# Kernel optimization log

Hardware: AMD Instinct MI355X
Metric: run time of the kernel (lower is better)

Reference implementation:

```python
import jax, jax.numpy as jnp
import numpy as np

B, N, F = 512, 32, 16          # batch graphs, nodes per graph, node_obs dim (last col = entity type)
H, E, NE, L = 128, 16, 3, 2    # hidden, embedding_size, num_embeddings, embed_layer_N
MAX_EDGE_DIST = 1.0


def layer_norm(x, g, b, eps=1e-5):
    mu = jnp.mean(x, axis=-1, keepdims=True)
    var = jnp.mean((x - mu) ** 2, axis=-1, keepdims=True)
    return (x - mu) / jnp.sqrt(var + eps) * g + b


def setup_inputs() -> dict:
    key = jax.random.key(0)
    ks = jax.random.split(key, 12)
    feats = jax.random.normal(ks[0], (B, N, F - 1), jnp.float32)
    ent = jax.random.randint(ks[1], (B, N), 0, NE).astype(jnp.float32)
    node_obs = jnp.concatenate([feats, ent[..., None]], axis=-1)
    adj = jax.random.uniform(ks[2], (B, N, N), jnp.float32, 0.0, 2.0)
    adj = adj * (1.0 - jnp.eye(N, dtype=jnp.float32))  # no self distance
    agent_id = jax.random.randint(ks[3], (B, 1), 0, N)
    D0 = (F - 1) + E + 1  # node feats + entity embed + edge_attr
    s = 0.05
    return dict(
        node_obs=node_obs, adj=adj, agent_id=agent_id,
        entity_embed=jax.random.normal(ks[4], (NE, E), jnp.float32) * s,
        lin1_w=jax.random.normal(ks[5], (D0, H), jnp.float32) * s, lin1_b=jnp.zeros(H, jnp.float32),
        ln1_g=jnp.ones(H, jnp.float32), ln1_b=jnp.zeros(H, jnp.float32),
        linh_w=jax.random.normal(ks[6], (L, H, H), jnp.float32) * s, linh_b=jnp.zeros((L, H), jnp.float32),
        lnh_g=jnp.ones((L, H), jnp.float32), lnh_b=jnp.zeros((L, H), jnp.float32),
        fc2a_w=jax.random.normal(ks[7], (H, H), jnp.float32) * s, fc2a_b=jnp.zeros(H, jnp.float32),
        fc2b_w=jax.random.normal(ks[8], (H, 1), jnp.float32) * s, fc2b_b=jnp.zeros(1, jnp.float32),
        fc3_w=jax.random.normal(ks[9], (H, H), jnp.float32) * s, fc3_b=jnp.zeros(H, jnp.float32),
        ln3_g=jnp.ones(H, jnp.float32), ln3_b=jnp.zeros(H, jnp.float32),
        fc4_w=jax.random.normal(ks[10], (H, H), jnp.float32) * s, fc4_b=jnp.zeros(H, jnp.float32),
        ln4_g=jnp.ones(H, jnp.float32), ln4_b=jnp.zeros(H, jnp.float32),
    )


def reference(node_obs, adj, agent_id, entity_embed,
              lin1_w, lin1_b, ln1_g, ln1_b,
              linh_w, linh_b, lnh_g, lnh_b,
              fc2a_w, fc2a_b, fc2b_w, fc2b_b,
              fc3_w, fc3_b, ln3_g, ln3_b,
              fc4_w, fc4_b, ln4_g, ln4_b):
    # processAdj: edge (r -> c) exists where 0 < adj[r,c] < max_edge_dist, edge_attr = adj value
    mask = ((adj > 0) & (adj < MAX_EDGE_DIST)).astype(adj.dtype)      # [B,N,N] (r=source, c=target)
    e = adj * mask
    # EmbedConv.message: x_j features + entity embedding + edge_attr -> MLP
    feat_j = node_obs[..., :-1]                                       # [B,N,F-1]
    ent = node_obs[..., -1].astype(jnp.int32)                         # [B,N]
    xj = jnp.concatenate([feat_j, entity_embed[ent]], axis=-1)        # [B,N,F-1+E]
    src = jnp.broadcast_to(xj[:, :, None, :], (B, N, N, xj.shape[-1]))
    pair = jnp.concatenate([src, e[..., None]], axis=-1)              # [B,r,c,D0]
    m = layer_norm(jax.nn.relu(pair @ lin1_w + lin1_b), ln1_g, ln1_b) # [B,r,c,H]
    for l in range(linh_w.shape[0]):
        m = layer_norm(jax.nn.relu(m @ linh_w[l] + linh_b[l]), lnh_g[l], lnh_b[l])
    # scatter-add aggregation at target node c (masked sum over sources r)
    h = jnp.einsum('brc,brch->bch', mask, m)                          # [B,N,H]
    hf = h.reshape(B * N, -1)
    # attention: fc2 then softmax over ALL batched-graph nodes (dim=0, as in source)
    alpha = jax.nn.softmax(jax.nn.relu(hf @ fc2a_w + fc2a_b) @ fc2b_w + fc2b_b, axis=0)  # [B*N,1]
    v = layer_norm(jax.nn.relu(hf @ fc3_w + fc3_b), ln3_g, ln3_b)
    x = layer_norm(jax.nn.relu((alpha * v) @ fc4_w + fc4_b), ln4_g, ln4_b)
    x = x.reshape(B, N, -1)
    # graph_aggr == 'node': gather agent's node features
    out = x[jnp.arange(B), agent_id[:, 0].astype(jnp.int32)]          # [B,H]
    return out
```

## Files before the change

### kernel.cpp

```cpp
#include <hip/hip_runtime.h>
#include <hip/hip_bf16.h>


typedef __attribute__((ext_vector_type(8))) __bf16 bf16x8;
typedef __attribute__((ext_vector_type(4))) float  f32x4;
typedef __attribute__((ext_vector_type(2))) float  f32x2;

__device__ float g_bf[256];

__device__ __forceinline__ unsigned short f2bf(float f) {
  union { float f; unsigned u; } v; v.f = f;
  unsigned u = v.u;
  u += 0x7FFFu + ((u >> 16) & 1u);
  return (unsigned short)(u >> 16);
}

__device__ __forceinline__ unsigned pk2bf(float a, float b) {
  union { __hip_bfloat162 h; unsigned u; } cv;
  cv.h = __float22bfloat162_rn(make_float2(a, b));
  return cv.u;
}

__device__ __forceinline__ bf16x8 lds_frag(const unsigned short* p) {
  union { uint4 u; bf16x8 v; } x;
  x.u = *(const uint4*)p;
  return x.v;
}

__device__ __forceinline__ f32x4 mfma16(bf16x8 a, bf16x8 b, f32x4 c) {
  return __builtin_amdgcn_mfma_f32_16x16x32_bf16(a, b, c, 0, 0, 0);
}

__device__ __forceinline__ float dpp_add16(float x) {
  union { float f; int i; } a, t;
  a.f = x;
  t.i = __builtin_amdgcn_update_dpp(0, a.i, 0xB1,  0xF, 0xF, true); a.f += t.f;
  t.i = __builtin_amdgcn_update_dpp(0, a.i, 0x4E,  0xF, 0xF, true); a.f += t.f;
  t.i = __builtin_amdgcn_update_dpp(0, a.i, 0x141, 0xF, 0xF, true); a.f += t.f;
  t.i = __builtin_amdgcn_update_dpp(0, a.i, 0x140, 0xF, 0xF, true); a.f += t.f;
  return a.f;
}

__device__ __forceinline__ void gll16(const void* g, void* l) {
  __builtin_amdgcn_global_load_lds(
      (const __attribute__((address_space(1))) unsigned int*)(unsigned long long)g,
      (__attribute__((address_space(3))) unsigned int*)(unsigned int)(unsigned long long)l,
      16, 0, 0);
}

__device__ __forceinline__ void stage18432(const char* g, char* l, int tid) {
  int off = tid * 16;
  gll16(g + off,         l + off);
  gll16(g + off + 4096,  l + off + 4096);
  gll16(g + off + 8192,  l + off + 8192);
  gll16(g + off + 12288, l + off + 12288);
  if (tid < 128) gll16(g + off + 16384, l + off + 16384);
}

#define WS_HB    0
#define WS_HSEL  4194304
#define WS_SWS   4456448
#define WS_STATS 4521984
#define WS_XJB   4522240
#define WS_WT0P  5570816
#define WS_W1P   5581056
#define WS_W2P   5617920
#define WS_WT3P  5654784

#define PREP_N0 524288
#define PREP_N1 (PREP_N0 + 5120)
#define PREP_N2 (PREP_N1 + 36864)
#define PREP_N3 (PREP_N2 + 17408)
#define PREP_N4 (PREP_N3 + 256)
#define PREP_N5 (PREP_N4 + 2)

__global__ void k_prep(const float* __restrict__ node_obs, const float* __restrict__ ent_emb,
                       const float* __restrict__ lin1_w, const float* __restrict__ linh_w,
                       const float* __restrict__ fc2a_w,
                       const float* __restrict__ ln1_g, const float* __restrict__ ln1_b,
                       const float* __restrict__ lnh_g, const float* __restrict__ lnh_b,
                       const float* __restrict__ linh_b,
                       char* __restrict__ ws) {
  int idx = blockIdx.x * 256 + threadIdx.x;
  unsigned short* xjb  = (unsigned short*)(ws + WS_XJB);
  unsigned short* WT0p = (unsigned short*)(ws + WS_WT0P);
  unsigned short* W1p  = (unsigned short*)(ws + WS_W1P);
  unsigned short* W2p  = (unsigned short*)(ws + WS_W2P);
  unsigned short* WT3p = (unsigned short*)(ws + WS_WT3P);
  if (idx < PREP_N0) {
    int row = idx >> 5, k = idx & 31;
    float val;
    if (k < 15) val = node_obs[row * 16 + k];
    else if (k < 31) {
      int ent = (int)node_obs[row * 16 + 15];
      val = ent_emb[ent * 16 + (k - 15)];
    } else val = 0.f;
    xjb[idx] = f2bf(val);
  } else if (idx < PREP_N1) {
    int r = idx - PREP_N0;
    int n = r / 40, kk = r - n * 40;
    WT0p[n * 40 + kk] = (kk < 32) ? f2bf(lin1_w[kk * 128 + n]) : (unsigned short)0;
  } else if (idx < PREP_N2) {
    int r = idx - PREP_N1;
    int l = r / 18432; r -= l * 18432;
    int h = r / 9216;  r -= h * 9216;
    int n = r / 72;    int kk = r - n * 72;
    unsigned short v = 0;
    if (kk < 64) {
      int p  = h * 64 + kk;
      int ok = 32 * (p >> 5) + 16 * (p & 1) + ((p >> 1) & 15);
      float g = l ? lnh_g[ok] : ln1_g[ok];
      v = f2bf(g * linh_w[l * 16384 + ok * 128 + n]);
    }
    (l ? W2p : W1p)[h * 9216 + n * 72 + kk] = v;
  } else if (idx < PREP_N3) {
    int r = idx - PREP_N2;
    int n = r / 136, kk = r - n * 136;
    unsigned short v = 0;
    if (kk < 128) {
      int ok = 32 * (kk >> 5) + 16 * (kk & 1) + ((kk >> 1) & 15);
      v = f2bf(fc2a_w[ok * 128 + n]);
    }
    WT3p[n * 136 + kk] = v;
  } else if (idx < PREP_N4) {
    int r = idx - PREP_N3;
    int which = r >> 7, n = r & 127;
    const float* be = which ? lnh_b : ln1_b;
    const float* w  = linh_w + which * 16384 + n;
    float a = linh_b[which * 128 + n];
#pragma unroll 8
    for (int k = 0; k < 128; ++k) a += be[k] * w[k * 128];
    g_bf[which * 128 + n] = a;
  } else if (idx < PREP_N5) {
    ((unsigned*)(ws + WS_STATS + 16))[idx - PREP_N4] = 0u;
  }
}

__global__ __launch_bounds__(256)
void k_mask(const float* __restrict__ adj, char* __restrict__ ws) {
  const int tid = threadIdx.x, lane = tid & 63, wv = tid >> 6;
  int p = blockIdx.x * 256 + tid;
  int b = p >> 5, c = p & 31;
  int cnt = 0;
#pragma unroll 8
  for (int r = 0; r < 32; ++r) {
    float a = adj[(b * 32 + r) * 32 + c];
    cnt += (a > 0.f && a < 1.f) ? 1 : 0;
  }
  const bool big = cnt > 16;
  unsigned long long bal = __ballot(big);
  __shared__ unsigned sb[4], ss[4];
  __shared__ unsigned base_b, base_s;
  if (lane == 0) {
    unsigned nb = (unsigned)__popcll(bal);
    sb[wv] = nb; ss[wv] = 64u - nb;
  }
  __syncthreads();
  if (tid == 0) {
    unsigned tb = 0, ts = 0;
#pragma unroll
    for (int i = 0; i < 4; ++i) {
      unsigned t = sb[i]; sb[i] = tb; tb += t;
      t = ss[i]; ss[i] = ts; ts += t;
    }
    unsigned* tcnt = (unsigned*)(ws + WS_STATS + 16);
    base_b = atomicAdd(&tcnt[0], tb);
    base_s = atomicAdd(&tcnt[1], ts);
  }
  __syncthreads();
  unsigned long long mlow = (1ull << lane) - 1ull;
  unsigned short* bigl = (unsigned short*)(ws + WS_SWS);
  unsigned short* smal = bigl + 16384;
  if (big) {
    unsigned rk = base_b + sb[wv] + (unsigned)__popcll(bal & mlow);
    bigl[rk] = (unsigned short)p;
  } else {
    unsigned rk = base_s + ss[wv] + (unsigned)__popcll(~bal & mlow);
    smal[rk] = (unsigned short)p;
  }
}

__device__ __forceinline__ void bias_acc(f32x4 (&acc)[2][8],
                                         const float* __restrict__ gb, int li) {
#pragma unroll
  for (int tj = 0; tj < 8; ++tj) {
    float b = gb[tj * 16 + li];
#pragma unroll
    for (int ti = 0; ti < 2; ++ti)
#pragma unroll
      for (int q = 0; q < 4; ++q) acc[ti][tj][q] = b;
  }
}

__device__ __forceinline__ void epilogue_store(f32x4 (&acc)[2][8],
    unsigned short* Xs, int wv, int li, int quad) {
  const f32x2 z2 = {0.f, 0.f};
#pragma unroll
  for (int ti = 0; ti < 2; ++ti) {
#pragma unroll
    for (int rp = 0; rp < 2; ++rp) {
      f32x2 vv[8], s1 = {0.f, 0.f}, s2 = {0.f, 0.f};
#pragma unroll
      for (int tj = 0; tj < 8; ++tj) {
        f32x2 x = { acc[ti][tj][2 * rp], acc[ti][tj][2 * rp + 1] };
        x = __builtin_elementwise_max(x, z2);
        vv[tj] = x; s1 += x; s2 += x * x;
      }
      f32x2 S1 = { dpp_add16(s1.x), dpp_add16(s1.y) };
      f32x2 S2 = { dpp_add16(s2.x), dpp_add16(s2.y) };
      f32x2 mean = S1 * 0.0078125f;
      f32x2 var  = S2 * 0.0078125f - mean * mean;
      f32x2 inv  = { rsqrtf(var.x + 1e-5f), rsqrtf(var.y + 1e-5f) };
      f32x2 c0   = -mean * inv;
      int r0 = 32 * wv + ti * 16 + quad * 4 + 2 * rp;
      unsigned* d0 = (unsigned*)(Xs + r0 * 136);
      unsigned* d1 = (unsigned*)(Xs + (r0 + 1) * 136);
#pragma unroll
      for (int g4 = 0; g4 < 4; ++g4) {
        f32x2 oa = vv[2 * g4]     * inv + c0;
        f32x2 ob = vv[2 * g4 + 1] * inv + c0;
        d0[g4 * 16 + li] = pk2bf(oa.x, ob.x);
        d1[g4 * 16 + li] = pk2bf(oa.y, ob.y);
      }
    }
  }
}

__device__ __forceinline__ void agg_reduce_write(float (&T)[8], float Q, float NM,
    const float* __restrict__ gg, const float* __restrict__ gbe,
    int pair, const int* __restrict__ agent_id, char* __restrict__ ws,
    int li, int quad) {
#pragma unroll
  for (int tj = 0; tj < 8; ++tj) {
    T[tj] += __shfl_xor(T[tj], 16);
    T[tj] += __shfl_xor(T[tj], 32);
  }
  Q += __shfl_xor(Q, 16); Q += __shfl_xor(Q, 32);
  if (quad != 0 || pair < 0) return;
  float cs[8];
#pragma unroll
  for (int tj = 0; tj < 8; ++tj) {
    int col = tj * 16 + li;
    cs[tj] = gg[col] * (T[tj] - Q) + NM * gbe[col];
  }
  unsigned* hb32 = (unsigned*)((unsigned short*)(ws + WS_HB) + pair * 128);
#pragma unroll
  for (int g4 = 0; g4 < 4; ++g4)
    hb32[g4 * 16 + li] = pk2bf(cs[2 * g4], cs[2 * g4 + 1]);
  int b = pair >> 5;
  if ((pair & 31) == agent_id[b]) {
    float* hs = (float*)(ws + WS_HSEL) + b * 128;
#pragma unroll
    for (int tj = 0; tj < 8; ++tj) hs[tj * 16 + li] = cs[tj];
  }
}

__device__ __forceinline__ void epilogue_agg2(f32x4 (&acc)[2][8],
    const float* __restrict__ gg, const float* __restrict__ gbe,
    int big, int cnt0, int cnt1, int p0, int p1,
    const int* __restrict__ agent_id, char* __restrict__ ws,
    int li, int quad) {
  const f32x2 z2 = {0.f, 0.f};
  float T0[8], T1[8], Q0 = 0.f, Q1 = 0.f;
#pragma unroll
  for (int ti = 0; ti < 2; ++ti) {
    f32x2 Tp[8];
#pragma unroll
    for (int tj = 0; tj < 8; ++tj) Tp[tj] = z2;
    f32x2 Qp = z2;
    float lim   = big ? (float)(cnt0 + cnt1) : (float)(ti ? cnt1 : cnt0);
    float rbase = (float)((big ? ti * 16 : 0) + quad * 4);
#pragma unroll
    for (int rp = 0; rp < 2; ++rp) {
      f32x2 vv[8], s1 = z2, s2 = z2;
#pragma unroll
      for (int tj = 0; tj < 8; ++tj) {
        f32x2 x = { acc[ti][tj][2 * rp], acc[ti][tj][2 * rp + 1] };
        x = __builtin_elementwise_max(x, z2);
        vv[tj] = x; s1 += x; s2 += x * x;
      }
      f32x2 S1 = { dpp_add16(s1.x), dpp_add16(s1.y) };
      f32x2 S2 = { dpp_add16(s2.x), dpp_add16(s2.y) };
      f32x2 mean = S1 * 0.0078125f;
      f32x2 var  = S2 * 0.0078125f - mean * mean;
      f32x2 inv  = { rsqrtf(var.x + 1e-5f), rsqrtf(var.y + 1e-5f) };
      float r0f = rbase + (float)(2 * rp);
      f32x2 mk = { (r0f < lim) ? 1.f : 0.f, (r0f + 1.f < lim) ? 1.f : 0.f };
      f32x2 u = mk * inv;
      Qp += u * mean;
#pragma unroll
      for (int tj = 0; tj < 8; ++tj) Tp[tj] += u * vv[tj];
    }
    if (ti == 0) {
#pragma unroll
      for (int tj = 0; tj < 8; ++tj) T0[tj] = Tp[tj].x + Tp[tj].y;
      Q0 = Qp.x + Qp.y;
    } else {
#pragma unroll
      for (int tj = 0; tj < 8; ++tj) T1[tj] = Tp[tj].x + Tp[tj].y;
      Q1 = Qp.x + Qp.y;
    }
  }
  if (big) {
#pragma unroll
    for (int tj = 0; tj < 8; ++tj) T0[tj] += T1[tj];
    Q0 += Q1;
    agg_reduce_write(T0, Q0, (float)(cnt0 + cnt1), gg, gbe, p0, agent_id, ws, li, quad);
  } else {
    agg_reduce_write(T0, Q0, (float)cnt0, gg, gbe, p0, agent_id, ws, li, quad);
    agg_reduce_write(T1, Q1, (float)cnt1, gg, gbe, p1, agent_id, ws, li, quad);
  }
}

#define SMP_W 34816
#define SMP_TOTAL 53248

__device__ __forceinline__ void mfma_half(f32x4 (&acc)[2][8],
    const unsigned short* Xs, const unsigned short* Wh,
    int xoff, int wv, int li, int quad) {
#pragma unroll
  for (int s = 0; s < 2; ++s) {
    bf16x8 a0 = lds_frag(Xs + (32 * wv + li) * 136 + xoff + s * 32 + quad * 8);
    bf16x8 a1 = lds_frag(Xs + (32 * wv + 16 + li) * 136 + xoff + s * 32 + quad * 8);
#pragma unroll
    for (int tj = 0; tj < 8; ++tj) {
      bf16x8 bb = lds_frag(Wh + (tj * 16 + li) * 72 + s * 32 + quad * 8);
      acc[0][tj] = mfma16(a0, bb, acc[0][tj]);
      acc[1][tj] = mfma16(a1, bb, acc[1][tj]);
    }
  }
}

__global__ __launch_bounds__(256, 3)
void k_pair(const float* __restrict__ adj, const int* __restrict__ agent_id,
            const float* __restrict__ lin1_b,
            const float* __restrict__ lnh_g, const float* __restrict__ lnh_b,
            char* __restrict__ ws) {
  __shared__ alignas(16) char smem[SMP_TOTAL];
  unsigned short* Xs = (unsigned short*)smem;
  unsigned short* Wh = (unsigned short*)(smem + SMP_W);

  const unsigned short* xjb = (const unsigned short*)(ws + WS_XJB);
  const char* WT0p = ws + WS_WT0P;
  const char* W1p  = ws + WS_W1P;
  const char* W2p  = ws + WS_W2P;

  const int tid  = threadIdx.x;
  const int lane = tid & 63, li = lane & 15, quad = lane >> 4, wv = tid >> 6;

  const unsigned* tcnt = (const unsigned*)(ws + WS_STATS + 16);
  const int n_big = (int)tcnt[0], n_small = (int)tcnt[1];
  const int n_task = n_big + ((n_small + 1) >> 1);
  if ((int)(blockIdx.x * 4) >= n_task) return;
  const int slot = blockIdx.x * 4 + wv;
  const unsigned short* bigl = (const unsigned short*)(ws + WS_SWS);
  const unsigned short* smal = bigl + 16384;
  int p0 = -1, p1 = -1, big = 0;
  if (slot < n_big) { p0 = bigl[slot]; big = 1; }
  else if (slot < n_task) {
    int j = slot - n_big;
    p0 = smal[2 * j];
    if (2 * j + 1 < n_small) p1 = smal[2 * j + 1];
  }

  const int r = lane & 31, hh = lane >> 5;
  int pp = big ? (hh ? -1 : p0) : (hh ? p1 : p0);
  float a_val = 0.f;
  if (pp >= 0) a_val = adj[(((pp >> 5) * 32 + r) * 32) + (pp & 31)];
  const bool live = (a_val > 0.f) && (a_val < 1.f);
  unsigned long long bal = __ballot(live);
  unsigned hm = hh ? (unsigned)(bal >> 32) : (unsigned)bal;
  int pre = __popc(hm & ((1u << r) - 1u));
  int slot_in = big ? pre : (hh * 16 + pre);
  int cnt0, cnt1;
  if (big) { int ca = __popc((unsigned)bal); cnt0 = ca < 16 ? ca : 16; cnt1 = ca - cnt0; }
  else     { cnt0 = __popc((unsigned)bal); cnt1 = __popc((unsigned)(bal >> 32)); }
  unsigned* scr = (unsigned*)(smem + 10240 + wv * 128);
  if (live) scr[slot_in] = (unsigned)r;

  {
    const uint4* src = (const uint4*)xjb;
    char* tile = smem + wv * 2560;
    int j0 = lane >> 2, j1 = 16 + (lane >> 2), pt = lane & 3;
    int ca = cnt0 + cnt1;
    bool v0 = j0 < (big ? ca : cnt0);
    bool v1 = big ? (j1 < ca) : ((j1 - 16) < cnt1);
    int b0 = (p0 < 0 ? 0 : p0 >> 5);
    int b1 = (p1 < 0 ? 0 : p1 >> 5);
    int sb1 = big ? b0 : b1;
    unsigned sr0 = v0 ? scr[j0] : 0u;
    unsigned sr1 = v1 ? scr[j1] : 0u;
    uint4 z4 = {0u, 0u, 0u, 0u};
    uint4 q0 = v0 ? src[(b0 * 32 + (int)sr0) * 4 + pt] : z4;
    uint4 q1 = v1 ? src[(sb1 * 32 + (int)sr1) * 4 + pt] : z4;
    *(uint4*)(tile + j0 * 80 + pt * 16) = q0;
    *(uint4*)(tile + j1 * 80 + pt * 16) = q1;
    if (live) ((unsigned short*)(tile + slot_in * 80))[31] = f2bf(a_val);
  }
  {
    int off = tid * 16;
    gll16(WT0p + off, smem + SMP_W + off);
    gll16(WT0p + off + 4096, smem + SMP_W + off + 4096);
    if (tid < 128) gll16(WT0p + off + 8192, smem + SMP_W + off + 8192);
  }
  __syncthreads();

  f32x4 acc[2][8];

  bias_acc(acc, lin1_b, li);
  {
    const unsigned short* xt = (const unsigned short*)(smem + wv * 2560);
    bf16x8 a0 = lds_frag(xt + li * 40 + quad * 8);
    bf16x8 a1 = lds_frag(xt + (li + 16) * 40 + quad * 8);
#pragma unroll
    for (int tj = 0; tj < 8; ++tj) {
      bf16x8 bb = lds_frag(Wh + (tj * 16 + li) * 40 + quad * 8);
      acc[0][tj] = mfma16(a0, bb, acc[0][tj]);
      acc[1][tj] = mfma16(a1, bb, acc[1][tj]);
    }
  }
  __syncthreads();
  stage18432(W1p, smem + SMP_W, tid);
  epilogue_store(acc, Xs, wv, li, quad);
  __syncthreads();

  bias_acc(acc, g_bf, li);
  mfma_half(acc, Xs, Wh, 0, wv, li, quad);
  __syncthreads();
  stage18432(W1p + 18432, smem + SMP_W, tid);
  __syncthreads();
  mfma_half(acc, Xs, Wh, 64, wv, li, quad);
  __syncthreads();
  stage18432(W2p, smem + SMP_W, tid);
  epilogue_store(acc, Xs, wv, li, quad);
  __syncthreads();

  bias_acc(acc, g_bf + 128, li);
  mfma_half(acc, Xs, Wh, 0, wv, li, quad);
  __syncthreads();
  stage18432(W2p + 18432, smem + SMP_W, tid);
  __syncthreads();
  mfma_half(acc, Xs, Wh, 64, wv, li, quad);

  epilogue_agg2(acc, lnh_g + 128, lnh_b + 128, big, cnt0, cnt1, p0, p1,
                agent_id, ws, li, quad);
}

#define SC_TOTAL 70656
__global__ __launch_bounds__(256, 2)
void k_score(const char* __restrict__ ws,
             const float* __restrict__ fc2a_b, const float* __restrict__ fc2b_w,
             const float* __restrict__ fc2b_b) {
  __shared__ alignas(16) char smem[SC_TOTAL];
  unsigned short* Xs = (unsigned short*)smem;
  unsigned short* Ws = (unsigned short*)(smem + 34816);
  float* P = (float*)(smem + 69632);
  const int tid = threadIdx.x;
  const int row0 = blockIdx.x * 128;
  const uint4* hb4 = (const uint4*)(ws + WS_HB);
  const char* WT3p = ws + WS_WT3P;
  float* sws = (float*)((char*)ws + WS_SWS);

  for (int i = tid; i < 2048; i += 256) {
    int row = i >> 4, ch = i & 15;
    uint4 v = hb4[(row0 + row) * 16 + ch];
    *(uint4*)(Xs + row * 136 + ch * 8) = v;
  }
  {
    int off = tid * 16;
#pragma unroll
    for (int it = 0; it < 8; ++it) gll16(WT3p + off + it * 4096, smem + 34816 + off + it * 4096);
    if (tid < 128) gll16(WT3p + off + 32768, smem + 34816 + off + 32768);
  }
  if (tid < 128) { P[tid] = fc2a_b[tid]; P[128 + tid] = fc2b_w[tid]; }
  __syncthreads();

  const int lane = tid & 63, li = lane & 15, quad = lane >> 4, wv = tid >> 6;
  f32x4 acc[2][8];
#pragma unroll
  for (int ti = 0; ti < 2; ++ti)
#pragma unroll
    for (int tj = 0; tj < 8; ++tj)
#pragma unroll
      for (int q = 0; q < 4; ++q) acc[ti][tj][q] = 0.f;
#pragma unroll
  for (int s = 0; s < 4; ++s) {
    bf16x8 a0 = lds_frag(Xs + (32 * wv + li) * 136 + s * 32 + quad * 8);
    bf16x8 a1 = lds_frag(Xs + (32 * wv + 16 + li) * 136 + s * 32 + quad * 8);
#pragma unroll
    for (int tj = 0; tj < 8; ++tj) {
      bf16x8 bb = lds_frag(Ws + (tj * 16 + li) * 136 + s * 32 + quad * 8);
      acc[0][tj] = mfma16(a0, bb, acc[0][tj]);
      acc[1][tj] = mfma16(a1, bb, acc[1][tj]);
    }
  }
  float bs[8], w2[8];
#pragma unroll
  for (int tj = 0; tj < 8; ++tj) {
    bs[tj] = P[tj * 16 + li];
    w2[tj] = P[128 + tj * 16 + li];
  }
  float b2 = fc2b_b[0];
#pragma unroll
  for (int ti = 0; ti < 2; ++ti) {
#pragma unroll
    for (int rg = 0; rg < 4; ++rg) {
      float t = 0.f;
#pragma unroll
      for (int tj = 0; tj < 8; ++tj) {
        float x = acc[ti][tj][rg] + bs[tj];
        x = fmaxf(x, 0.f);
        t += x * w2[tj];
      }
#pragma unroll
      for (int m = 1; m < 16; m <<= 1) t += __shfl_xor(t, m);
      if (li == 0) sws[row0 + 32 * wv + ti * 16 + quad * 4 + rg] = t + b2;
    }
  }
}

__global__ __launch_bounds__(1024)
void k_stats(char* __restrict__ ws) {
  const float* sws = (const float*)(ws + WS_SWS);
  float* stats = (float*)(ws + WS_STATS);
  __shared__ float red[1024];
  const int tid = threadIdx.x;
  float m = -3.0e38f;
  for (int i = tid; i < 16384; i += 1024) m = fmaxf(m, sws[i]);
  red[tid] = m;
  __syncthreads();
  for (int st = 512; st > 0; st >>= 1) {
    if (tid < st) red[tid] = fmaxf(red[tid], red[tid + st]);
    __syncthreads();
  }
  float mx = red[0];
  __syncthreads();
  float sm = 0.f;
  for (int i = tid; i < 16384; i += 1024) sm += __expf(sws[i] - mx);
  red[tid] = sm;
  __syncthreads();
  for (int st = 512; st > 0; st >>= 1) {
    if (tid < st) red[tid] += red[tid + st];
    __syncthreads();
  }
  if (tid == 0) { stats[0] = mx; stats[1] = red[0]; }
}

__global__ __launch_bounds__(128)
void k_final(const char* __restrict__ ws, const int* __restrict__ agent_id,
             const float* __restrict__ fc3_w, const float* __restrict__ fc3_b,
             const float* __restrict__ ln3_g, const float* __restrict__ ln3_b,
             const float* __restrict__ fc4_w, const float* __restrict__ fc4_b,
             const float* __restrict__ ln4_g, const float* __restrict__ ln4_b,
             float* __restrict__ out) {
  const float* hsel  = (const float*)(ws + WS_HSEL);
  const float* sws   = (const float*)(ws + WS_SWS);
  const float* stats = (const float*)(ws + WS_STATS);
  __shared__ float xrow[128];
  __shared__ float red[8];
  const int tid = threadIdx.x;
  const int b = blockIdx.x;
  xrow[tid] = hsel[b * 128 + tid];
  __syncthreads();
  float t = fc3_b[tid];
  for (int k = 0; k < 128; ++k) t += xrow[k] * fc3_w[k * 128 + tid];
  t = fmaxf(t, 0.f);
  float s1 = t, s2 = t * t;
#pragma unroll
  for (int m = 1; m < 64; m <<= 1) { s1 += __shfl_xor(s1, m); s2 += __shfl_xor(s2, m); }
  if ((tid & 63) == 0) { red[(tid >> 6) * 2] = s1; red[(tid >> 6) * 2 + 1] = s2; }
  __syncthreads();
  s1 = red[0] + red[2]; s2 = red[1] + red[3];
  float mean = s1 * 0.0078125f;
  float var  = s2 * 0.0078125f - mean * mean;
  float inv  = rsqrtf(var + 1e-5f);
  float v = (t - mean) * inv * ln3_g[tid] + ln3_b[tid];
  float alpha = __expf(sws[b * 32 + agent_id[b]] - stats[0]) / stats[1];
  __syncthreads();
  xrow[tid] = alpha * v;
  __syncthreads();
  float x = fc4_b[tid];
  for (int k = 0; k < 128; ++k) x += xrow[k] * fc4_w[k * 128 + tid];
  x = fmaxf(x, 0.f);
  s1 = x; s2 = x * x;
#pragma unroll
  for (int m = 1; m < 64; m <<= 1) { s1 += __shfl_xor(s1, m); s2 += __shfl_xor(s2, m); }
  if ((tid & 63) == 0) { red[4 + (tid >> 6) * 2] = s1; red[5 + (tid >> 6) * 2] = s2; }
  __syncthreads();
  s1 = red[4] + red[6]; s2 = red[5] + red[7];
  mean = s1 * 0.0078125f;
  var  = s2 * 0.0078125f - mean * mean;
  inv  = rsqrtf(var + 1e-5f);
  out[b * 128 + tid] = (x - mean) * inv * ln4_g[tid] + ln4_b[tid];
}

extern "C" void kernel_launch(void* const* d_in, const int* in_sizes, int n_in,
                              void* d_out, int out_size, void* d_ws, size_t ws_size,
                              hipStream_t stream) {
  (void)in_sizes; (void)n_in; (void)out_size; (void)ws_size;
  const float* node_obs = (const float*)d_in[0];
  const float* adj      = (const float*)d_in[1];
  const int*   agent_id = (const int*)d_in[2];
  const float* ent_emb  = (const float*)d_in[3];
  const float* lin1_w   = (const float*)d_in[4];
  const float* lin1_b   = (const float*)d_in[5];
  const float* ln1_g    = (const float*)d_in[6];
  const float* ln1_beta = (const float*)d_in[7];
  const float* linh_w   = (const float*)d_in[8];
  const float* linh_b   = (const float*)d_in[9];
  const float* lnh_g    = (const float*)d_in[10];
  const float* lnh_b    = (const float*)d_in[11];
  const float* fc2a_b   = (const float*)d_in[13];
  const float* fc2b_w   = (const float*)d_in[14];
  const float* fc2b_b   = (const float*)d_in[15];
  const float* fc3_w    = (const float*)d_in[16];
  const float* fc3_b    = (const float*)d_in[17];
  const float* ln3_g    = (const float*)d_in[18];
  const float* ln3_b    = (const float*)d_in[19];
  const float* fc4_w    = (const float*)d_in[20];
  const float* fc4_b    = (const float*)d_in[21];
  const float* ln4_g    = (const float*)d_in[22];
  const float* ln4_b    = (const float*)d_in[23];
  float* out = (float*)d_out;
  char* ws = (char*)d_ws;

  k_prep<<<(PREP_N5 + 255) / 256, 256, 0, stream>>>(node_obs, ent_emb, lin1_w, linh_w,
                                                    (const float*)d_in[12],
                                                    ln1_g, ln1_beta, lnh_g, lnh_b,
                                                    linh_b, ws);
  k_mask<<<64, 256, 0, stream>>>(adj, ws);
  k_pair<<<4096, 256, 0, stream>>>(adj, agent_id, lin1_b, lnh_g, lnh_b, ws);
  k_score<<<128, 256, 0, stream>>>(ws, fc2a_b, fc2b_w, fc2b_b);
  k_stats<<<1, 1024, 0, stream>>>(ws);
  k_final<<<512, 128, 0, stream>>>(ws, agent_id,
                                   fc3_w, fc3_b, ln3_g, ln3_b,
                                   fc4_w, fc4_b, ln4_g, ln4_b, out);
}
```

Baseline: 188.7 us.

## Make k_pair persistent with all MLP weights resident in LDS

k_pair becomes a persistent kernel: 256 blocks of 512 threads loop over tasks with a grid-stride loop. The three layer weight matrices are loaded into LDS once per block instead of being restaged in halves for every task. Each wave gets its own activation buffer, which removes the block-wide barriers between layers. Biases and LayerNorm parameters are hoisted into registers. The cost is about 154 KB of LDS per block, so only one block (8 waves) fits per CU, and load balancing relies on the grid stride.

```diff
diff --git a/kernel.cpp b/kernel.cpp
--- a/kernel.cpp
+++ b/kernel.cpp
@@ -46,15 +46,6 @@
       (const __attribute__((address_space(1))) unsigned int*)(unsigned long long)g,
       (__attribute__((address_space(3))) unsigned int*)(unsigned int)(unsigned long long)l,
       16, 0, 0);
-}
-
-__device__ __forceinline__ void stage18432(const char* g, char* l, int tid) {
-  int off = tid * 16;
-  gll16(g + off,         l + off);
-  gll16(g + off + 4096,  l + off + 4096);
-  gll16(g + off + 8192,  l + off + 8192);
-  gll16(g + off + 12288, l + off + 12288);
-  if (tid < 128) gll16(g + off + 16384, l + off + 16384);
 }
 
 #define WS_HB    0
@@ -180,20 +171,17 @@
   }
 }
 
-__device__ __forceinline__ void bias_acc(f32x4 (&acc)[2][8],
-                                         const float* __restrict__ gb, int li) {
-#pragma unroll
-  for (int tj = 0; tj < 8; ++tj) {
-    float b = gb[tj * 16 + li];
+__device__ __forceinline__ void bias_acc(f32x4 (&acc)[2][8], const float (&b8)[8]) {
+#pragma unroll
+  for (int tj = 0; tj < 8; ++tj)
 #pragma unroll
     for (int ti = 0; ti < 2; ++ti)
 #pragma unroll
-      for (int q = 0; q < 4; ++q) acc[ti][tj][q] = b;
-  }
+      for (int q = 0; q < 4; ++q) acc[ti][tj][q] = b8[tj];
 }
 
 __device__ __forceinline__ void epilogue_store(f32x4 (&acc)[2][8],
-    unsigned short* Xs, int wv, int li, int quad) {
+    unsigned short* Xw, int li, int quad) {
   const f32x2 z2 = {0.f, 0.f};
 #pragma unroll
   for (int ti = 0; ti < 2; ++ti) {
@@ -212,9 +200,9 @@
       f32x2 var  = S2 * 0.0078125f - mean * mean;
       f32x2 inv  = { rsqrtf(var.x + 1e-5f), rsqrtf(var.y + 1e-5f) };
       f32x2 c0   = -mean * inv;
-      int r0 = 32 * wv + ti * 16 + quad * 4 + 2 * rp;
-      unsigned* d0 = (unsigned*)(Xs + r0 * 136);
-      unsigned* d1 = (unsigned*)(Xs + (r0 + 1) * 136);
+      int r0 = ti * 16 + quad * 4 + 2 * rp;
+      unsigned* d0 = (unsigned*)(Xw + r0 * 136);
+      unsigned* d1 = (unsigned*)(Xw + (r0 + 1) * 136);
 #pragma unroll
       for (int g4 = 0; g4 < 4; ++g4) {
         f32x2 oa = vv[2 * g4]     * inv + c0;
@@ -227,7 +215,7 @@
 }
 
 __device__ __forceinline__ void agg_reduce_write(float (&T)[8], float Q, float NM,
-    const float* __restrict__ gg, const float* __restrict__ gbe,
+    const float (&gg8)[8], const float (&be8)[8],
     int pair, const int* __restrict__ agent_id, char* __restrict__ ws,
     int li, int quad) {
 #pragma unroll
@@ -239,10 +227,8 @@
   if (quad != 0 || pair < 0) return;
   float cs[8];
 #pragma unroll
-  for (int tj = 0; tj < 8; ++tj) {
-    int col = tj * 16 + li;
-    cs[tj] = gg[col] * (T[tj] - Q) + NM * gbe[col];
-  }
+  for (int tj = 0; tj < 8; ++tj)
+    cs[tj] = gg8[tj] * (T[tj] - Q) + NM * be8[tj];
   unsigned* hb32 = (unsigned*)((unsigned short*)(ws + WS_HB) + pair * 128);
 #pragma unroll
   for (int g4 = 0; g4 < 4; ++g4)
@@ -256,7 +242,7 @@
 }
 
 __device__ __forceinline__ void epilogue_agg2(f32x4 (&acc)[2][8],
-    const float* __restrict__ gg, const float* __restrict__ gbe,
+    const float (&gg8)[8], const float (&be8)[8],
     int big, int cnt0, int cnt1, int p0, int p1,
     const int* __restrict__ agent_id, char* __restrict__ ws,
     int li, int quad) {
@@ -305,145 +291,148 @@
 #pragma unroll
     for (int tj = 0; tj < 8; ++tj) T0[tj] += T1[tj];
     Q0 += Q1;
-    agg_reduce_write(T0, Q0, (float)(cnt0 + cnt1), gg, gbe, p0, agent_id, ws, li, quad);
+    agg_reduce_write(T0, Q0, (float)(cnt0 + cnt1), gg8, be8, p0, agent_id, ws, li, quad);
   } else {
-    agg_reduce_write(T0, Q0, (float)cnt0, gg, gbe, p0, agent_id, ws, li, quad);
-    agg_reduce_write(T1, Q1, (float)cnt1, gg, gbe, p1, agent_id, ws, li, quad);
-  }
-}
-
-#define SMP_W 34816
-#define SMP_TOTAL 53248
-
-__device__ __forceinline__ void mfma_half(f32x4 (&acc)[2][8],
-    const unsigned short* Xs, const unsigned short* Wh,
-    int xoff, int wv, int li, int quad) {
-#pragma unroll
-  for (int s = 0; s < 2; ++s) {
-    bf16x8 a0 = lds_frag(Xs + (32 * wv + li) * 136 + xoff + s * 32 + quad * 8);
-    bf16x8 a1 = lds_frag(Xs + (32 * wv + 16 + li) * 136 + xoff + s * 32 + quad * 8);
+    agg_reduce_write(T0, Q0, (float)cnt0, gg8, be8, p0, agent_id, ws, li, quad);
+    agg_reduce_write(T1, Q1, (float)cnt1, gg8, be8, p1, agent_id, ws, li, quad);
+  }
+}
+
+#define PL_W0    0
+#define PL_W1    10240
+#define PL_W2    47104
+#define PL_XS    83968
+#define PL_SCR   153600
+#define PL_TOTAL 154624
+
+__device__ __forceinline__ void mfma_fullK(f32x4 (&acc)[2][8],
+    const unsigned short* Xw, const unsigned short* Wl, int li, int quad) {
+#pragma unroll
+  for (int s = 0; s < 4; ++s) {
+    const unsigned short* Wh = Wl + (s >> 1) * 9216;
+    const int ko = (s & 1) * 32 + quad * 8;
+    bf16x8 a0 = lds_frag(Xw + li * 136 + s * 32 + quad * 8);
+    bf16x8 a1 = lds_frag(Xw + (16 + li) * 136 + s * 32 + quad * 8);
 #pragma unroll
     for (int tj = 0; tj < 8; ++tj) {
-      bf16x8 bb = lds_frag(Wh + (tj * 16 + li) * 72 + s * 32 + quad * 8);
+      bf16x8 bb = lds_frag(Wh + (tj * 16 + li) * 72 + ko);
       acc[0][tj] = mfma16(a0, bb, acc[0][tj]);
       acc[1][tj] = mfma16(a1, bb, acc[1][tj]);
     }
   }
 }
 
-__global__ __launch_bounds__(256, 3)
+__global__ __launch_bounds__(512, 2)
 void k_pair(const float* __restrict__ adj, const int* __restrict__ agent_id,
             const float* __restrict__ lin1_b,
             const float* __restrict__ lnh_g, const float* __restrict__ lnh_b,
             char* __restrict__ ws) {
-  __shared__ alignas(16) char smem[SMP_TOTAL];
-  unsigned short* Xs = (unsigned short*)smem;
-  unsigned short* Wh = (unsigned short*)(smem + SMP_W);
-
-  const unsigned short* xjb = (const unsigned short*)(ws + WS_XJB);
-  const char* WT0p = ws + WS_WT0P;
-  const char* W1p  = ws + WS_W1P;
-  const char* W2p  = ws + WS_W2P;
-
+  __shared__ alignas(16) char smem[PL_TOTAL];
   const int tid  = threadIdx.x;
   const int lane = tid & 63, li = lane & 15, quad = lane >> 4, wv = tid >> 6;
+
+  {
+    const char* g = ws + WS_WT0P;
+    int off = tid * 16;
+#pragma unroll
+    for (int i = 0; i < 10; ++i) gll16(g + off + i * 8192, smem + off + i * 8192);
+    if (tid < 128) gll16(g + off + 81920, smem + off + 81920);
+  }
 
   const unsigned* tcnt = (const unsigned*)(ws + WS_STATS + 16);
   const int n_big = (int)tcnt[0], n_small = (int)tcnt[1];
   const int n_task = n_big + ((n_small + 1) >> 1);
-  if ((int)(blockIdx.x * 4) >= n_task) return;
-  const int slot = blockIdx.x * 4 + wv;
   const unsigned short* bigl = (const unsigned short*)(ws + WS_SWS);
   const unsigned short* smal = bigl + 16384;
-  int p0 = -1, p1 = -1, big = 0;
-  if (slot < n_big) { p0 = bigl[slot]; big = 1; }
-  else if (slot < n_task) {
-    int j = slot - n_big;
-    p0 = smal[2 * j];
-    if (2 * j + 1 < n_small) p1 = smal[2 * j + 1];
-  }
+  const unsigned short* xjb  = (const unsigned short*)(ws + WS_XJB);
+
+  unsigned short* Xw = (unsigned short*)(smem + PL_XS + wv * 8704);
+  unsigned*      scr = (unsigned*)(smem + PL_SCR + wv * 128);
+  const unsigned short* W0 = (const unsigned short*)(smem + PL_W0);
+  const unsigned short* W1 = (const unsigned short*)(smem + PL_W1);
+  const unsigned short* W2 = (const unsigned short*)(smem + PL_W2);
+
+  float b0_[8], b1_[8], b2_[8], gg8[8], be8[8];
+#pragma unroll
+  for (int tj = 0; tj < 8; ++tj) {
+    int col = tj * 16 + li;
+    b0_[tj] = lin1_b[col];
+    b1_[tj] = g_bf[col];
+    b2_[tj] = g_bf[128 + col];
+    gg8[tj] = lnh_g[128 + col];
+    be8[tj] = lnh_b[128 + col];
+  }
+
+  __syncthreads();
 
   const int r = lane & 31, hh = lane >> 5;
-  int pp = big ? (hh ? -1 : p0) : (hh ? p1 : p0);
-  float a_val = 0.f;
-  if (pp >= 0) a_val = adj[(((pp >> 5) * 32 + r) * 32) + (pp & 31)];
-  const bool live = (a_val > 0.f) && (a_val < 1.f);
-  unsigned long long bal = __ballot(live);
-  unsigned hm = hh ? (unsigned)(bal >> 32) : (unsigned)bal;
-  int pre = __popc(hm & ((1u << r) - 1u));
-  int slot_in = big ? pre : (hh * 16 + pre);
-  int cnt0, cnt1;
-  if (big) { int ca = __popc((unsigned)bal); cnt0 = ca < 16 ? ca : 16; cnt1 = ca - cnt0; }
-  else     { cnt0 = __popc((unsigned)bal); cnt1 = __popc((unsigned)(bal >> 32)); }
-  unsigned* scr = (unsigned*)(smem + 10240 + wv * 128);
-  if (live) scr[slot_in] = (unsigned)r;
-
-  {
-    const uint4* src = (const uint4*)xjb;
-    char* tile = smem + wv * 2560;
-    int j0 = lane >> 2, j1 = 16 + (lane >> 2), pt = lane & 3;
-    int ca = cnt0 + cnt1;
-    bool v0 = j0 < (big ? ca : cnt0);
-    bool v1 = big ? (j1 < ca) : ((j1 - 16) < cnt1);
-    int b0 = (p0 < 0 ? 0 : p0 >> 5);
-    int b1 = (p1 < 0 ? 0 : p1 >> 5);
-    int sb1 = big ? b0 : b1;
-    unsigned sr0 = v0 ? scr[j0] : 0u;
-    unsigned sr1 = v1 ? scr[j1] : 0u;
-    uint4 z4 = {0u, 0u, 0u, 0u};
-    uint4 q0 = v0 ? src[(b0 * 32 + (int)sr0) * 4 + pt] : z4;
-    uint4 q1 = v1 ? src[(sb1 * 32 + (int)sr1) * 4 + pt] : z4;
-    *(uint4*)(tile + j0 * 80 + pt * 16) = q0;
-    *(uint4*)(tile + j1 * 80 + pt * 16) = q1;
-    if (live) ((unsigned short*)(tile + slot_in * 80))[31] = f2bf(a_val);
-  }
-  {
-    int off = tid * 16;
-    gll16(WT0p + off, smem + SMP_W + off);
-    gll16(WT0p + off + 4096, smem + SMP_W + off + 4096);
-    if (tid < 128) gll16(WT0p + off + 8192, smem + SMP_W + off + 8192);
-  }
-  __syncthreads();
-
-  f32x4 acc[2][8];
-
-  bias_acc(acc, lin1_b, li);
-  {
-    const unsigned short* xt = (const unsigned short*)(smem + wv * 2560);
-    bf16x8 a0 = lds_frag(xt + li * 40 + quad * 8);
-    bf16x8 a1 = lds_frag(xt + (li + 16) * 40 + quad * 8);
-#pragma unroll
-    for (int tj = 0; tj < 8; ++tj) {
-      bf16x8 bb = lds_frag(Wh + (tj * 16 + li) * 40 + quad * 8);
-      acc[0][tj] = mfma16(a0, bb, acc[0][tj]);
-      acc[1][tj] = mfma16(a1, bb, acc[1][tj]);
-    }
-  }
-  __syncthreads();
-  stage18432(W1p, smem + SMP_W, tid);
-  epilogue_store(acc, Xs, wv, li, quad);
-  __syncthreads();
-
-  bias_acc(acc, g_bf, li);
-  mfma_half(acc, Xs, Wh, 0, wv, li, quad);
-  __syncthreads();
-  stage18432(W1p + 18432, smem + SMP_W, tid);
-  __syncthreads();
-  mfma_half(acc, Xs, Wh, 64, wv, li, quad);
-  __syncthreads();
-  stage18432(W2p, smem + SMP_W, tid);
-  epilogue_store(acc, Xs, wv, li, quad);
-  __syncthreads();
-
-  bias_acc(acc, g_bf + 128, li);
-  mfma_half(acc, Xs, Wh, 0, wv, li, quad);
-  __syncthreads();
-  stage18432(W2p + 18432, smem + SMP_W, tid);
-  __syncthreads();
-  mfma_half(acc, Xs, Wh, 64, wv, li, quad);
-
-  epilogue_agg2(acc, lnh_g + 128, lnh_b + 128, big, cnt0, cnt1, p0, p1,
-                agent_id, ws, li, quad);
+
+  for (int slot = (int)blockIdx.x * 8 + wv; slot < n_task; slot += 2048) {
+    int p0, p1 = -1, big = 0;
+    if (slot < n_big) { p0 = bigl[slot]; big = 1; }
+    else {
+      int j = slot - n_big;
+      p0 = smal[2 * j];
+      p1 = (2 * j + 1 < n_small) ? smal[2 * j + 1] : -1;
+    }
+
+    int pp = big ? (hh ? -1 : p0) : (hh ? p1 : p0);
+    float a_val = 0.f;
+    if (pp >= 0) a_val = adj[(((pp >> 5) * 32 + r) * 32) + (pp & 31)];
+    const bool live = (a_val > 0.f) && (a_val < 1.f);
+    unsigned long long bal = __ballot(live);
+    unsigned hm = hh ? (unsigned)(bal >> 32) : (unsigned)bal;
+    int pre = __popc(hm & ((1u << r) - 1u));
+    int slot_in = big ? pre : (hh * 16 + pre);
+    int cnt0, cnt1;
+    if (big) { int ca = __popc((unsigned)bal); cnt0 = ca < 16 ? ca : 16; cnt1 = ca - cnt0; }
+    else     { cnt0 = __popc((unsigned)bal); cnt1 = __popc((unsigned)(bal >> 32)); }
+    if (live) scr[slot_in] = (unsigned)r;
+
+    {
+      const uint4* src = (const uint4*)xjb;
+      char* tile = (char*)Xw;
+      int j0 = lane >> 2, j1 = 16 + (lane >> 2), pt = lane & 3;
+      int ca = cnt0 + cnt1;
+      bool v0 = j0 < (big ? ca : cnt0);
+      bool v1 = big ? (j1 < ca) : ((j1 - 16) < cnt1);
+      int b0 = (p0 < 0 ? 0 : p0 >> 5);
+      int b1 = (p1 < 0 ? 0 : p1 >> 5);
+      int sb1 = big ? b0 : b1;
+      unsigned sr0 = v0 ? scr[j0] : 0u;
+      unsigned sr1 = v1 ? scr[j1] : 0u;
+      uint4 z4 = {0u, 0u, 0u, 0u};
+      uint4 q0 = v0 ? src[(b0 * 32 + (int)sr0) * 4 + pt] : z4;
+      uint4 q1 = v1 ? src[(sb1 * 32 + (int)sr1) * 4 + pt] : z4;
+      *(uint4*)(tile + j0 * 80 + pt * 16) = q0;
+      *(uint4*)(tile + j1 * 80 + pt * 16) = q1;
+      if (live) ((unsigned short*)(tile + slot_in * 80))[31] = f2bf(a_val);
+    }
+
+    f32x4 acc[2][8];
+
+    bias_acc(acc, b0_);
+    {
+      const unsigned short* xt = Xw;
+      bf16x8 a0 = lds_frag(xt + li * 40 + quad * 8);
+      bf16x8 a1 = lds_frag(xt + (li + 16) * 40 + quad * 8);
+#pragma unroll
+      for (int tj = 0; tj < 8; ++tj) {
+        bf16x8 bb = lds_frag(W0 + (tj * 16 + li) * 40 + quad * 8);
+        acc[0][tj] = mfma16(a0, bb, acc[0][tj]);
+        acc[1][tj] = mfma16(a1, bb, acc[1][tj]);
+      }
+    }
+    epilogue_store(acc, Xw, li, quad);
+
+    bias_acc(acc, b1_);
+    mfma_fullK(acc, Xw, W1, li, quad);
+    epilogue_store(acc, Xw, li, quad);
+
+    bias_acc(acc, b2_);
+    mfma_fullK(acc, Xw, W2, li, quad);
+    epilogue_agg2(acc, gg8, be8, big, cnt0, cnt1, p0, p1, agent_id, ws, li, quad);
+  }
 }
 
 #define SC_TOTAL 70656
@@ -629,7 +618,7 @@
                                                     ln1_g, ln1_beta, lnh_g, lnh_b,
                                                     linh_b, ws);
   k_mask<<<64, 256, 0, stream>>>(adj, ws);
-  k_pair<<<4096, 256, 0, stream>>>(adj, agent_id, lin1_b, lnh_g, lnh_b, ws);
+  k_pair<<<256, 512, 0, stream>>>(adj, agent_id, lin1_b, lnh_g, lnh_b, ws);
   k_score<<<128, 256, 0, stream>>>(ws, fc2a_b, fc2b_w, fc2b_b);
   k_stats<<<1, 1024, 0, stream>>>(ws);
   k_final<<<512, 128, 0, stream>>>(ws, agent_id,
```

Result: slower. 193.4 us (+2.5%).
